# Performance work log

Hardware: AMD Instinct MI355X
Metric: run time of the kernel (lower is better)

Reference implementation:

```python
import jax, jax.numpy as jnp
import numpy as np

KS, AS = 13, 12  # kernel_size (12 vertices + center), anchor_size (icosahedron vertices)


def _icosa():
    # Icosahedron oriented with vertex 0 on +z (required by sort_level_vs xy-rotation logic)
    r5 = np.sqrt(5.0); rr = 2.0 / r5
    vs = [[0.0, 0.0, 1.0]]
    for k in range(5):
        t = 2.0 * np.pi * k / 5.0
        vs.append([rr * np.cos(t), rr * np.sin(t), 1.0 / r5])
    for k in range(5):
        t = 2.0 * np.pi * k / 5.0 + np.pi / 5.0
        vs.append([rr * np.cos(t), rr * np.sin(t), -1.0 / r5])
    vs.append([0.0, 0.0, -1.0])
    return np.array(vs)


def _rotm(axis, ang):
    a = np.asarray(axis, dtype=np.float64); a = a / np.linalg.norm(a)
    K = np.array([[0, -a[2], a[1]], [a[2], 0, -a[0]], [-a[1], a[0], 0]])
    return np.eye(3) + np.sin(ang) * K + (1.0 - np.cos(ang)) * (K @ K)


def _ico_group(vs):
    # Generate the 60-element icosahedral rotation group by closure from two generators
    gens = [_rotm([0.0, 0.0, 1.0], 2 * np.pi / 5), _rotm(vs[1], 2 * np.pi / 5)]
    group = [np.eye(3)]
    keys = {tuple(np.round(np.eye(3), 4).ravel())}
    frontier = [np.eye(3)]
    while frontier:
        nxt = []
        for g in frontier:
            for h in gens:
                c = h @ g
                k = tuple(np.round(c, 4).ravel())
                if k not in keys:
                    keys.add(k); group.append(c); nxt.append(c)
        frontier = nxt
    return group


def _sort_level_vs(v_idxs, vs):
    # Faithful port of sort_level_vs: order ring vertices by successive 72-deg xy rotations
    out = [v_idxs[0]]
    vs_l = vs[v_idxs][:, :2]
    cur = vs_l[[0]]
    dth = 2 * np.pi / 5
    R = np.array([[np.cos(dth), -np.sin(dth)], [np.sin(dth), np.cos(dth)]])
    for _ in range(4):
        cur = R.dot(cur.T).T
        out.append(v_idxs[np.argmin(np.abs(vs_l - cur).sum(1))])
    return np.array(out)


def _build_buffers():
    vs = _icosa()
    dots = vs @ vs.T
    v0_adjs = np.where(np.abs(dots[0] - 1.0 / np.sqrt(5)) < 1e-6)[0]
    v0_lv2 = np.where(np.abs(dots[0] + 1.0 / np.sqrt(5)) < 1e-6)[0]
    v0_opp = int(np.argmin(dots[0]))
    # 12 rotation anchors: one group element mapping vertex 0 to each vertex
    group = _ico_group(vs)
    vRs = []
    for i in range(12):
        for R in group:
            if np.linalg.norm(R @ vs[0] - vs[i]) < 1e-5:
                vRs.append(R); break
    vRs = np.stack(vRs)  # [12,3,3]
    rot_v = np.einsum('rij,aj->rai', vRs, vs)  # [12,12,3]
    d = np.linalg.norm(rot_v[:, :, None, :] - vs[None, None], axis=-1)
    trace_idx_ori = np.argmin(d, axis=2)  # [12,12] vertex permutation per anchor rotation
    trace_idx_rot = np.empty_like(trace_idx_ori)
    for r in range(12):
        trace_idx_rot[r, trace_idx_ori[r]] = np.arange(12)
    trace_idxv_rot = np.concatenate([trace_idx_rot, np.full((12, 1), 12, np.int64)], axis=1)  # [12,13]
    # idx_map: faithful port of the __init__ construction (maps 13*12 slots -> 36 weight params)
    inv = np.empty(12, np.int64)
    inv[0] = 0; inv[v0_adjs] = 1; inv[v0_lv2] = 2; inv[v0_opp] = 3
    a_s = _sort_level_vs(v0_adjs, vs)
    l_s = _sort_level_vs(v0_lv2, vs)
    idx_map = np.empty(KS * AS, np.int64)
    idx_map[:AS] = inv
    idx_map[v0_opp * AS:(v0_opp + 1) * AS] = inv + 4
    idx_map[-AS:] = inv + 8
    seq1 = np.arange(12, 24); seq2 = np.arange(24, 36)
    idx_map[a_s[0] * AS:(a_s[0] + 1) * AS] = seq1
    idx_map[l_s[0] * AS:(l_s[0] + 1) * AS] = seq2
    shifts = [[4, 0, 1, 2, 3], [3, 4, 0, 1, 2], [2, 3, 4, 0, 1], [1, 2, 3, 4, 0]]
    for j, sh in enumerate(shifts, start=1):
        new = np.empty(12, np.int64)
        new[a_s] = a_s[sh]; new[l_s] = l_s[sh]
        new[0] = 0; new[v0_opp] = v0_opp
        idx_map[a_s[j] * AS:(a_s[j] + 1) * AS] = seq1[new]
        idx_map[l_s[j] * AS:(l_s[j] + 1) * AS] = seq2[new]
    return idx_map, trace_idxv_rot, trace_idx_rot


def setup_inputs() -> dict:
    key = jax.random.key(0)
    k1, k2 = jax.random.split(key)
    B, CIN, COUT, P = 8, 16, 16, 4096
    x = jax.random.normal(k1, (B, CIN, KS, P, AS), dtype=jnp.float32)
    W = jax.random.normal(k2, (COUT, CIN, 36), dtype=jnp.float32) * 0.05  # xavier-scale
    idx_map, tivr, tir = _build_buffers()
    return {
        'x': x,
        'W': W,
        'idx_map': jnp.asarray(idx_map, jnp.int32),
        'trace_idxv_rot': jnp.asarray(tivr, jnp.int32),
        'trace_idx_rot': jnp.asarray(tir, jnp.int32),
    }


def reference(x, W, idx_map, trace_idxv_rot, trace_idx_rot):
    d_out, d_in, _ = W.shape
    # Expand 36 free params to the [d, c, k, a] kernel via idx_map gather
    Wm = W[:, :, idx_map].reshape(d_out, d_in, KS, AS)
    # The two torch.gather calls (dims 2 then 3) collapse to:
    # Wfull[d,c,k,a,r] = Wm[d,c, trace_idxv_rot[r,k], trace_idx_rot[r,a]]
    Wfull = Wm[:, :, trace_idxv_rot[:, :, None], trace_idx_rot[:, None, :]]  # [d,c,r,k,a]
    return jnp.einsum('dcrka,bckpa->bdpr', Wfull, x)
```

## Files before the change

kernel.cpp:

```cpp
#include <hip/hip_runtime.h>

#define B_    8
#define CIN_  16
#define COUT_ 16
#define KS_   13
#define AS_   12
#define P_    4096
#define R_    12
#define M_    192
#define KTOT  2496
#define BN    128
#define KT    96
#define NSTEP 26
#define LDP   104

typedef float  f32x4  __attribute__((ext_vector_type(4)));
typedef __bf16 bf16x4 __attribute__((ext_vector_type(4)));
typedef __bf16 bf16x8 __attribute__((ext_vector_type(8)));

__global__ void build_wmat(const float* __restrict__ W,
                           const int* __restrict__ idx_map,
                           const int* __restrict__ tivr,
                           const int* __restrict__ tir,
                           __bf16* __restrict__ Wmat) {
  int m = blockIdx.x;
  int d = m / R_;
  int r = m - d * R_;
  for (int kap = threadIdx.x; kap < KTOT; kap += blockDim.x) {
    int c = kap / (KS_ * AS_);
    int t = kap - c * (KS_ * AS_);
    int k = t / AS_;
    int a = t - k * AS_;
    int s = idx_map[tivr[r * KS_ + k] * AS_ + tir[r * AS_ + a]];
    Wmat[m * KTOT + kap] = (__bf16)W[(d * CIN_ + c) * 36 + s];
  }
}

__global__ __launch_bounds__(512, 2)
void s2conv(const float* __restrict__ x,
            const __bf16* __restrict__ Wmat,
            float* __restrict__ out) {
  __shared__ __bf16 Ws[M_][LDP];
  __shared__ __bf16 Xs[BN][LDP];

  const int tid  = threadIdx.x;
  const int lane = tid & 63;
  const int wave = tid >> 6;
  const int wm   = wave >> 2;
  const int wn   = wave & 3;
  const int l15  = lane & 15;
  const int l4   = lane >> 4;

  const int wg = blockIdx.x;
  const int b  = wg >> 5;
  const int p0 = (wg & 31) << 7;

  f32x4 acc[6][2];
#pragma unroll
  for (int i = 0; i < 6; ++i)
#pragma unroll
    for (int j = 0; j < 2; ++j)
      acc[i][j] = f32x4{0.f, 0.f, 0.f, 0.f};

  auto load_x = [&](int kt, f32x4 (&st)[6]) {
    int ck = kt * 8 + wave;
    const f32x4* bp =
        (const f32x4*)(x + (size_t)(b * 208 + ck) * 49152 + (size_t)p0 * 12);
#pragma unroll
    for (int it = 0; it < 6; ++it) st[it] = bp[it * 64 + lane];
  };

  auto load_w = [&](int kt, bf16x8 (&wst)[5]) {
    const char* wb = (const char*)Wmat + (size_t)kt * (KT * 2);
#pragma unroll
    for (int j = 0; j < 5; ++j) {
      int i = tid + j * 512;
      if (i < 2304) {
        int row = i / 12;
        int chunk = i - row * 12;
        wst[j] = *(const bf16x8*)(wb + (size_t)row * (KTOT * 2) + chunk * 16);
      }
    }
  };

  auto write_tiles = [&](f32x4 (&st)[6], bf16x8 (&wst)[5]) {
#pragma unroll
    for (int j = 0; j < 5; ++j) {
      int i = tid + j * 512;
      if (i < 2304) {
        int row = i / 12;
        int chunk = i - row * 12;
        *(bf16x8*)((char*)&Ws[0][0] + row * (LDP * 2) + chunk * 16) = wst[j];
      }
    }
#pragma unroll
    for (int it = 0; it < 6; ++it) {
      int f4i = it * 64 + lane;
      int pl  = f4i / 3;
      int a   = (f4i - pl * 3) * 4;
      bf16x4 v = __builtin_convertvector(st[it], bf16x4);
      *(bf16x4*)((char*)&Xs[0][0] + pl * (LDP * 2) + (wave * 12 + a) * 2) = v;
    }
  };

  auto mfma_step = [&]() {
#pragma unroll
    for (int ks = 0; ks < 3; ++ks) {
      const int col = ks * 32 + l4 * 8;
      bf16x8 af[6], bfr[2];
#pragma unroll
      for (int mt = 0; mt < 6; ++mt)
        af[mt] = *(const bf16x8*)&Ws[wm * 96 + mt * 16 + l15][col];
#pragma unroll
      for (int nt = 0; nt < 2; ++nt)
        bfr[nt] = *(const bf16x8*)&Xs[wn * 32 + nt * 16 + l15][col];
#pragma unroll
      for (int mt = 0; mt < 6; ++mt)
#pragma unroll
        for (int nt = 0; nt < 2; ++nt)
          acc[mt][nt] = __builtin_amdgcn_mfma_f32_16x16x32_bf16(
              af[mt], bfr[nt], acc[mt][nt], 0, 0, 0);
    }
  };

  auto barrier1 = [&]() { __builtin_amdgcn_s_barrier(); };
  auto barrier2 = [&]() {
    asm volatile("s_waitcnt lgkmcnt(0)" ::: "memory");
    __builtin_amdgcn_s_barrier();
    __builtin_amdgcn_sched_barrier(0);
  };

  f32x4  stA[6], stB[6];
  bf16x8 wstA[5], wstB[5];
  load_x(0, stA); load_w(0, wstA);
  load_x(1, stB); load_w(1, wstB);

  for (int kt = 0; kt < NSTEP; kt += 2) {
    barrier1();
    write_tiles(stA, wstA);
    barrier2();
    if (kt + 2 < NSTEP) { load_x(kt + 2, stA); load_w(kt + 2, wstA); }
    mfma_step();

    barrier1();
    write_tiles(stB, wstB);
    barrier2();
    if (kt + 3 < NSTEP) { load_x(kt + 3, stB); load_w(kt + 3, wstB); }
    mfma_step();
  }

#pragma unroll
  for (int mt = 0; mt < 6; ++mt) {
    int mrow0 = wm * 96 + mt * 16 + l4 * 4;
    int d  = mrow0 / 12;
    int r0 = mrow0 - d * 12;
#pragma unroll
    for (int nt = 0; nt < 2; ++nt) {
      int p = p0 + wn * 32 + nt * 16 + l15;
      float* dst = out + (size_t)((b * 16 + d) * 4096 + p) * 12 + r0;
      *(f32x4*)dst = acc[mt][nt];
    }
  }
}

extern "C" void kernel_launch(void* const* d_in, const int* in_sizes, int n_in,
                              void* d_out, int out_size, void* d_ws, size_t ws_size,
                              hipStream_t stream) {
  const float* x       = (const float*)d_in[0];
  const float* W       = (const float*)d_in[1];
  const int*   idx_map = (const int*)d_in[2];
  const int*   tivr    = (const int*)d_in[3];
  const int*   tir     = (const int*)d_in[4];
  float*       out     = (float*)d_out;
  __bf16*      Wmat    = (__bf16*)d_ws;

  build_wmat<<<dim3(M_), dim3(256), 0, stream>>>(W, idx_map, tivr, tir, Wmat);
  s2conv<<<dim3(256), dim3(512), 0, stream>>>(x, Wmat, out);
}
```

Before: 82.58 us.

## Double-buffer LDS tiles to cut per-step barriers to one

Allocates two LDS buffers each for the weight and input tiles and restructures the main loop. While the MFMAs consume the current buffer, the next step's registers are written into the other buffer, and the global loads run two steps ahead. This removes one of the two workgroup barriers per K-step and lets LDS writes overlap with matrix math. The cost is doubled LDS use (roughly 133KB), which limits each CU to one workgroup; that matches the 256-block grid. It also drops the explicit scheduling barrier.

```diff
diff --git a/kernel.cpp b/kernel.cpp
--- a/kernel.cpp
+++ b/kernel.cpp
@@ -40,8 +40,8 @@
 void s2conv(const float* __restrict__ x,
             const __bf16* __restrict__ Wmat,
             float* __restrict__ out) {
-  __shared__ __bf16 Ws[M_][LDP];
-  __shared__ __bf16 Xs[BN][LDP];
+  __shared__ __bf16 Ws[2][M_][LDP];
+  __shared__ __bf16 Xs[2][BN][LDP];
 
   const int tid  = threadIdx.x;
   const int lane = tid & 63;
@@ -83,14 +83,16 @@
     }
   };
 
-  auto write_tiles = [&](f32x4 (&st)[6], bf16x8 (&wst)[5]) {
+  auto write_tiles = [&](int buf, f32x4 (&st)[6], bf16x8 (&wst)[5]) {
+    char* wsb = (char*)&Ws[buf][0][0];
+    char* xsb = (char*)&Xs[buf][0][0];
 #pragma unroll
     for (int j = 0; j < 5; ++j) {
       int i = tid + j * 512;
       if (i < 2304) {
         int row = i / 12;
         int chunk = i - row * 12;
-        *(bf16x8*)((char*)&Ws[0][0] + row * (LDP * 2) + chunk * 16) = wst[j];
+        *(bf16x8*)(wsb + row * (LDP * 2) + chunk * 16) = wst[j];
       }
     }
 #pragma unroll
@@ -99,21 +101,23 @@
       int pl  = f4i / 3;
       int a   = (f4i - pl * 3) * 4;
       bf16x4 v = __builtin_convertvector(st[it], bf16x4);
-      *(bf16x4*)((char*)&Xs[0][0] + pl * (LDP * 2) + (wave * 12 + a) * 2) = v;
+      *(bf16x4*)(xsb + pl * (LDP * 2) + (wave * 12 + a) * 2) = v;
     }
   };
 
-  auto mfma_step = [&]() {
+  auto mfma_step = [&](int buf) {
+    const __bf16* wsb = &Ws[buf][0][0];
+    const __bf16* xsb = &Xs[buf][0][0];
 #pragma unroll
     for (int ks = 0; ks < 3; ++ks) {
       const int col = ks * 32 + l4 * 8;
       bf16x8 af[6], bfr[2];
 #pragma unroll
       for (int mt = 0; mt < 6; ++mt)
-        af[mt] = *(const bf16x8*)&Ws[wm * 96 + mt * 16 + l15][col];
+        af[mt] = *(const bf16x8*)(wsb + (wm * 96 + mt * 16 + l15) * LDP + col);
 #pragma unroll
       for (int nt = 0; nt < 2; ++nt)
-        bfr[nt] = *(const bf16x8*)&Xs[wn * 32 + nt * 16 + l15][col];
+        bfr[nt] = *(const bf16x8*)(xsb + (wn * 32 + nt * 16 + l15) * LDP + col);
 #pragma unroll
       for (int mt = 0; mt < 6; ++mt)
 #pragma unroll
@@ -123,30 +127,29 @@
     }
   };
 
-  auto barrier1 = [&]() { __builtin_amdgcn_s_barrier(); };
-  auto barrier2 = [&]() {
+  auto barrier = [&]() {
     asm volatile("s_waitcnt lgkmcnt(0)" ::: "memory");
     __builtin_amdgcn_s_barrier();
-    __builtin_amdgcn_sched_barrier(0);
+  };
+
+  auto body = [&](int kt, f32x4 (&stI)[6], bf16x8 (&wstI)[5],
+                  f32x4 (&stW)[6], bf16x8 (&wstW)[5]) {
+    if (kt + 2 < NSTEP) { load_x(kt + 2, stI); load_w(kt + 2, wstI); }
+    if (kt + 1 < NSTEP) write_tiles(1 - (kt & 1), stW, wstW);
+    mfma_step(kt & 1);
+    barrier();
   };
 
   f32x4  stA[6], stB[6];
   bf16x8 wstA[5], wstB[5];
   load_x(0, stA); load_w(0, wstA);
   load_x(1, stB); load_w(1, wstB);
+  write_tiles(0, stA, wstA);
+  barrier();
 
   for (int kt = 0; kt < NSTEP; kt += 2) {
-    barrier1();
-    write_tiles(stA, wstA);
-    barrier2();
-    if (kt + 2 < NSTEP) { load_x(kt + 2, stA); load_w(kt + 2, wstA); }
-    mfma_step();
-
-    barrier1();
-    write_tiles(stB, wstB);
-    barrier2();
-    if (kt + 3 < NSTEP) { load_x(kt + 3, stB); load_w(kt + 3, wstB); }
-    mfma_step();
+    body(kt,     stA, wstA, stB, wstB);
+    body(kt + 1, stB, wstB, stA, wstA);
   }
 
 #pragma unroll
```

Result: slower. 84.92 us (+2.8%).
